# Kernel optimization log

Hardware: AMD Instinct MI355X
Metric: run time of the kernel (lower is better)

## Reference

```python
import jax, jax.numpy as jnp
import numpy as np

V, T, D, H, L, F, B = 50257, 1024, 1024, 16, 10, 4096, 2
HD = D // H  # head_dim = 64
EPS = 1e-5


def sinusoidal_pos(seq_len, d_model):
    pos = np.arange(seq_len)[:, None].astype(np.float32)
    i = np.arange(d_model // 2).astype(np.float32)
    inv = 1.0 / (10000.0 ** (2.0 * i / d_model))
    ang = pos * inv[None, :]
    pe = np.zeros((seq_len, d_model), dtype=np.float32)
    pe[:, 0::2] = np.sin(ang)
    pe[:, 1::2] = np.cos(ang)
    return jnp.asarray(pe)


def setup_inputs() -> dict:
    key = jax.random.key(0)
    ks = jax.random.split(key, 16)
    s = 0.02
    return {
        "x": jax.random.randint(ks[0], (B, T), 0, V),
        "emb": jax.random.normal(ks[1], (V, D), jnp.float32) * s,
        "pos": sinusoidal_pos(T, D),
        "Wq": jax.random.normal(ks[2], (L, D, D), jnp.float32) * s,
        "bq": jnp.zeros((L, D), jnp.float32),
        "Wk": jax.random.normal(ks[3], (L, D, D), jnp.float32) * s,
        "bk": jnp.zeros((L, D), jnp.float32),
        "Wv": jax.random.normal(ks[4], (L, D, D), jnp.float32) * s,
        "bv": jnp.zeros((L, D), jnp.float32),
        "ln_g": jnp.ones((L, D), jnp.float32),
        "ln_b": jnp.zeros((L, D), jnp.float32),
        "W1": jax.random.normal(ks[5], (L, D, F), jnp.float32) * s,
        "b1": jnp.zeros((L, F), jnp.float32),
        "W2": jax.random.normal(ks[6], (L, F, D), jnp.float32) * s,
        "b2": jnp.zeros((L, D), jnp.float32),
        "lnf_g": jnp.ones((D,), jnp.float32),
        "lnf_b": jnp.zeros((D,), jnp.float32),
        "Wout": jax.random.normal(ks[7], (D, V), jnp.float32) * s,
        "bout": jnp.zeros((V,), jnp.float32),
    }


def layer_norm(h, g, b):
    mu = jnp.mean(h, axis=-1, keepdims=True)
    var = jnp.mean(jnp.square(h - mu), axis=-1, keepdims=True)
    return (h - mu) * jax.lax.rsqrt(var + EPS) * g + b


def reference(x, emb, pos, Wq, bq, Wk, bk, Wv, bv, ln_g, ln_b, W1, b1, W2, b2, lnf_g, lnf_b, Wout, bout):
    t = x.shape[1]
    h = emb[x] + pos[None, :t]  # [B,T,D]
    causal = jnp.tril(jnp.ones((t, t), bool))  # True = keep
    scale = 1.0 / jnp.sqrt(jnp.float32(HD))

    def body(h, p):
        wq, bq_, wk, bk_, wv, bv_, g, bln, w1, b1_, w2, b2_ = p
        q = (h @ wq + bq_).reshape(B, t, H, HD)
        k = (h @ wk + bk_).reshape(B, t, H, HD)
        v = (h @ wv + bv_).reshape(B, t, H, HD)
        score = jnp.einsum('bqhd,bkhd->bhqk', q, k) * scale
        score = jnp.where(causal, score, -jnp.inf)
        attn = jax.nn.softmax(score, axis=-1)
        o = jnp.einsum('bhqk,bkhd->bqhd', attn, v).reshape(B, t, D)
        h = layer_norm(h + o, g, bln)
        m = jax.nn.gelu(h @ w1 + b1_, approximate=False) @ w2 + b2_
        h = layer_norm(h + m, g, bln)  # same LayerNorm params reused, as in source
        return h, None

    h, _ = jax.lax.scan(body, h, (Wq, bq, Wk, bk, Wv, bv, ln_g, ln_b, W1, b1, W2, b2))
    h = layer_norm(h, lnf_g, lnf_b)
    return h @ Wout + bout  # [B,T,V]
```

## Files before the change

### kernel.cpp

```cpp
#include <hip/hip_runtime.h>
#include <cstdint>
#include <cstddef>

#define Vv 50257
#define Va 50304
#define Tt 1024
#define Dd 1024
#define Hh 16
#define Ll 10
#define Ff 4096
#define Bb 2
#define Mm (Bb*Tt)

typedef float f32x4 __attribute__((ext_vector_type(4)));
typedef __bf16 bf16x8 __attribute__((ext_vector_type(8)));
typedef unsigned short u16x8 __attribute__((ext_vector_type(8)));
typedef unsigned short u16x4 __attribute__((ext_vector_type(4)));

static __device__ __forceinline__ unsigned short f2bf(float f) {
  unsigned int u = __builtin_bit_cast(unsigned int, f);
  unsigned int r = (u + 0x7FFFu + ((u >> 16) & 1u)) >> 16;
  return (unsigned short)r;
}

static __device__ __forceinline__ f32x4 mfma16x16x32(u16x8 a, u16x8 b, f32x4 c) {
  return __builtin_amdgcn_mfma_f32_16x16x32_bf16(
      __builtin_bit_cast(bf16x8, a), __builtin_bit_cast(bf16x8, b), c, 0, 0, 0);
}

static __device__ __forceinline__ void async_cp16(const void* g, void* l) {
  __builtin_amdgcn_global_load_lds(
      (const __attribute__((address_space(1))) unsigned int*)g,
      (__attribute__((address_space(3))) unsigned int*)l, 16, 0, 0);
}

__global__ __launch_bounds__(256) void embed_kernel(
    const int* __restrict__ x, const float* __restrict__ emb,
    const float* __restrict__ pos, float* __restrict__ h,
    unsigned short* __restrict__ hb) {
  int bt = blockIdx.x;
  int t = bt & (Tt - 1);
  int tok = x[bt];
  int i = threadIdx.x * 4;
  f32x4 e = *(const f32x4*)(emb + (size_t)tok * Dd + i);
  f32x4 p = *(const f32x4*)(pos + (size_t)t * Dd + i);
  f32x4 r = e + p;
  *(f32x4*)(h + (size_t)bt * Dd + i) = r;
  u16x4 rb = { f2bf(r[0]), f2bf(r[1]), f2bf(r[2]), f2bf(r[3]) };
  *(u16x4*)(hb + (size_t)bt * Dd + i) = rb;
}

__global__ __launch_bounds__(256) void add_ln_kernel(
    const float* __restrict__ hin, const float* __restrict__ r,
    const float* __restrict__ g, const float* __restrict__ bb,
    float* __restrict__ hout, unsigned short* __restrict__ hbout) {
  int row = blockIdx.x;
  int tid = threadIdx.x;
  size_t off = (size_t)row * Dd + tid * 4;
  f32x4 xv = *(const f32x4*)(hin + off);
  if (r) xv += *(const f32x4*)(r + off);
  float s  = xv[0] + xv[1] + xv[2] + xv[3];
  float ss = xv[0]*xv[0] + xv[1]*xv[1] + xv[2]*xv[2] + xv[3]*xv[3];
  #pragma unroll
  for (int o = 1; o < 64; o <<= 1) {
    s  += __shfl_xor(s, o);
    ss += __shfl_xor(ss, o);
  }
  __shared__ float red[8];
  int wave = tid >> 6, lane = tid & 63;
  if (lane == 0) { red[wave] = s; red[4 + wave] = ss; }
  __syncthreads();
  s  = red[0] + red[1] + red[2] + red[3];
  ss = red[4] + red[5] + red[6] + red[7];
  float mu = s * (1.0f / Dd);
  float var = ss * (1.0f / Dd) - mu * mu;
  float rstd = rsqrtf(var + 1e-5f);
  f32x4 gv = *(const f32x4*)(g + tid * 4);
  f32x4 bv = *(const f32x4*)(bb + tid * 4);
  f32x4 y;
  #pragma unroll
  for (int j = 0; j < 4; ++j) y[j] = (xv[j] - mu) * rstd * gv[j] + bv[j];
  *(f32x4*)(hout + off) = y;
  u16x4 yb = { f2bf(y[0]), f2bf(y[1]), f2bf(y[2]), f2bf(y[3]) };
  *(u16x4*)(hbout + off) = yb;
}

__global__ __launch_bounds__(256) void bias_gather_kernel(
    const float* __restrict__ bq, const float* __restrict__ bk,
    const float* __restrict__ bv, float* __restrict__ cb) {
  int l = blockIdx.x;
  int i = threadIdx.x * 4;
  f32x4 q = *(const f32x4*)(bq + (size_t)l * Dd + i);
  f32x4 k = *(const f32x4*)(bk + (size_t)l * Dd + i);
  f32x4 v = *(const f32x4*)(bv + (size_t)l * Dd + i);
  *(f32x4*)(cb + (size_t)l * 3072 + i) = q;
  *(f32x4*)(cb + (size_t)l * 3072 + 1024 + i) = k;
  *(f32x4*)(cb + (size_t)l * 3072 + 2048 + i) = v;
}

__global__ __launch_bounds__(256) void tconv_kernel(
    const float* __restrict__ W, unsigned short* __restrict__ Wt,
    int K, int N, int Nvalid, size_t sW, size_t sWt) {
  const float* Wl = W + (size_t)blockIdx.z * sW;
  unsigned short* Wtl = Wt + (size_t)blockIdx.z * sWt;
  __shared__ unsigned short t[64][72];
  int n0 = blockIdx.x * 64, k0 = blockIdx.y * 64;
  int tx = threadIdx.x & 15, ty = threadIdx.x >> 4;
  #pragma unroll
  for (int i = 0; i < 4; ++i) {
    int kr = ty + i * 16;
    int nc = tx * 4;
    int gn = n0 + nc;
    f32x4 v = {0.f, 0.f, 0.f, 0.f};
    if (gn + 3 < Nvalid) {
      v = *(const f32x4*)(Wl + (size_t)(k0 + kr) * N + gn);
    } else {
      #pragma unroll
      for (int j = 0; j < 4; ++j)
        if (gn + j < Nvalid) v[j] = Wl[(size_t)(k0 + kr) * N + gn + j];
    }
    t[nc + 0][kr] = f2bf(v[0]); t[nc + 1][kr] = f2bf(v[1]);
    t[nc + 2][kr] = f2bf(v[2]); t[nc + 3][kr] = f2bf(v[3]);
  }
  __syncthreads();
  #pragma unroll
  for (int i = 0; i < 4; ++i) {
    int nr = ty + i * 16;
    u16x4 o = *(const u16x4*)&t[nr][tx * 4];
    *(u16x4*)(Wtl + (size_t)(n0 + nr) * K + k0 + tx * 4) = o;
  }
}

template <int BM, int BN, int WR, int WC, int EPI, bool SWZ>
__global__ __launch_bounds__(256) void gemm_bt(
    const unsigned short* __restrict__ A, const unsigned short* __restrict__ Bt,
    const float* __restrict__ bias, void* __restrict__ Cout,
    int Ncols, int K) {
  static_assert(WR * WC == 4, "4 waves");
  constexpr int MI = BM / WR / 16;
  constexpr int NJ = BN / WC / 16;
  __shared__ __align__(16) unsigned short Al[2][BM * 32];
  __shared__ __align__(16) unsigned short Bl[2][BN * 32];
  int bx = blockIdx.x, by = blockIdx.y;
  if constexpr (SWZ) {
    unsigned gx = gridDim.x;
    unsigned total = gx * gridDim.y;
    unsigned flat = by * gx + bx;
    unsigned per = total >> 3;
    unsigned work = (flat & 7u) * per + (flat >> 3);
    bx = work % gx; by = work / gx;
  }
  const int bm = bx * BM;
  const int bn = by * BN;
  const int tid = threadIdx.x, lane = tid & 63, wave = tid >> 6;
  const int wm = (wave / WC) * (BM / WR);
  const int wn = (wave % WC) * (BN / WC);
  const int rowi = lane >> 2;
  const int koff = (lane & 3) * 8;

  auto stage = [&](int buf, int k0) {
    #pragma unroll
    for (int i = 0; i < BM / 64; ++i) {
      int ch = wave + i * 4;
      async_cp16(A + (size_t)(bm + ch * 16 + rowi) * K + k0 + koff, &Al[buf][ch * 512]);
    }
    #pragma unroll
    for (int i = 0; i < BN / 64; ++i) {
      int ch = wave + i * 4;
      async_cp16(Bt + (size_t)(bn + ch * 16 + rowi) * K + k0 + koff, &Bl[buf][ch * 512]);
    }
  };

  f32x4 acc[MI][NJ];
  #pragma unroll
  for (int i = 0; i < MI; ++i)
    #pragma unroll
    for (int j = 0; j < NJ; ++j) acc[i][j] = {0.f, 0.f, 0.f, 0.f};

  stage(0, 0);
  __syncthreads();
  int cur = 0;
  for (int k0 = 0; k0 < K; k0 += 32) {
    if (k0 + 32 < K) stage(cur ^ 1, k0 + 32);
    u16x8 af[MI], bfr[NJ];
    #pragma unroll
    for (int i = 0; i < MI; ++i)
      af[i] = *(const u16x8*)&Al[cur][(wm + i * 16 + (lane & 15)) * 32 + (lane >> 4) * 8];
    #pragma unroll
    for (int j = 0; j < NJ; ++j)
      bfr[j] = *(const u16x8*)&Bl[cur][(wn + j * 16 + (lane & 15)) * 32 + (lane >> 4) * 8];
    #pragma unroll
    for (int i = 0; i < MI; ++i)
      #pragma unroll
      for (int j = 0; j < NJ; ++j)
        acc[i][j] = mfma16x16x32(af[i], bfr[j], acc[i][j]);
    __syncthreads();
    cur ^= 1;
  }

  float bvv[NJ];
  #pragma unroll
  for (int j = 0; j < NJ; ++j) {
    int col = bn + wn + j * 16 + (lane & 15);
    bvv[j] = (col < Ncols) ? bias[col] : 0.0f;
  }
  #pragma unroll
  for (int i = 0; i < MI; ++i) {
    #pragma unroll
    for (int rr = 0; rr < 4; ++rr) {
      int row = bm + wm + i * 16 + (lane >> 4) * 4 + rr;
      #pragma unroll
      for (int j = 0; j < NJ; ++j) {
        int col = bn + wn + j * 16 + (lane & 15);
        if (col < Ncols) {
          float val = acc[i][j][rr] + bvv[j];
          if constexpr (EPI == 0) {
            ((float*)Cout)[(size_t)row * Ncols + col] = val;
          } else if constexpr (EPI == 1) {
            ((unsigned short*)Cout)[(size_t)row * Ncols + col] = f2bf(val);
          } else {
            float gv = 0.5f * val * (1.0f + erff(val * 0.70710678f));
            ((unsigned short*)Cout)[(size_t)row * Ncols + col] = f2bf(gv);
          }
        }
      }
    }
  }
}

template <int EPI>
__global__ __launch_bounds__(256) void gemm_f32b(
    const unsigned short* __restrict__ A, const float* __restrict__ Bw,
    const float* __restrict__ bias, void* __restrict__ Cout, int N, int K) {
  __shared__ __align__(16) unsigned short Al[128][40];
  __shared__ __align__(16) unsigned short Btl[128][40];
  const int bn = blockIdx.x * 128;
  const int bm = blockIdx.y * 128;
  const int tid = threadIdx.x;
  const int lane = tid & 63;
  const int wave = tid >> 6;
  const int wm = (wave >> 1) * 64;
  const int wn = (wave & 1) * 64;
  const bool nfast = ((N & 3) == 0);

  f32x4 acc[4][4];
  #pragma unroll
  for (int i = 0; i < 4; ++i)
    #pragma unroll
    for (int j = 0; j < 4; ++j) acc[i][j] = {0.f, 0.f, 0.f, 0.f};

  for (int k0 = 0; k0 < K; k0 += 32) {
    __syncthreads();
    #pragma unroll
    for (int i = 0; i < 2; ++i) {
      int c = tid + i * 256;
      int row = c >> 2, ko = (c & 3) * 8;
      u16x8 v = *(const u16x8*)(A + (size_t)(bm + row) * K + k0 + ko);
      *(u16x8*)&Al[row][ko] = v;
    }
    if (nfast) {
      #pragma unroll
      for (int i = 0; i < 4; ++i) {
        int c = tid + i * 256;
        int kr = c >> 5;
        int no = (c & 31) * 4;
        f32x4 v4 = *(const f32x4*)(Bw + (size_t)(k0 + kr) * N + bn + no);
        Btl[no + 0][kr] = f2bf(v4[0]); Btl[no + 1][kr] = f2bf(v4[1]);
        Btl[no + 2][kr] = f2bf(v4[2]); Btl[no + 3][kr] = f2bf(v4[3]);
      }
    } else {
      #pragma unroll
      for (int i = 0; i < 4; ++i) {
        int c = tid + i * 256;
        int kr = c >> 5;
        int nb = c & 31;
        #pragma unroll
        for (int j = 0; j < 4; ++j) {
          int col = nb + j * 32;
          float v = (bn + col < N) ? Bw[(size_t)(k0 + kr) * N + bn + col] : 0.0f;
          Btl[col][kr] = f2bf(v);
        }
      }
    }
    __syncthreads();
    u16x8 af[4], bfr[4];
    #pragma unroll
    for (int i = 0; i < 4; ++i)
      af[i] = *(const u16x8*)&Al[wm + i * 16 + (lane & 15)][(lane >> 4) * 8];
    #pragma unroll
    for (int j = 0; j < 4; ++j)
      bfr[j] = *(const u16x8*)&Btl[wn + j * 16 + (lane & 15)][(lane >> 4) * 8];
    #pragma unroll
    for (int i = 0; i < 4; ++i)
      #pragma unroll
      for (int j = 0; j < 4; ++j)
        acc[i][j] = mfma16x16x32(af[i], bfr[j], acc[i][j]);
  }
  #pragma unroll
  for (int j = 0; j < 4; ++j) {
    int col = bn + wn + j * 16 + (lane & 15);
    bool cok = (col < N);
    float bv = cok ? bias[col] : 0.0f;
    #pragma unroll
    for (int i = 0; i < 4; ++i) {
      #pragma unroll
      for (int rr = 0; rr < 4; ++rr) {
        int row = bm + wm + i * 16 + (lane >> 4) * 4 + rr;
        float val = acc[i][j][rr] + bv;
        if (cok) {
          if constexpr (EPI == 0) ((float*)Cout)[(size_t)row * N + col] = val;
          else if constexpr (EPI == 1) ((unsigned short*)Cout)[(size_t)row * N + col] = f2bf(val);
          else {
            float gv = 0.5f * val * (1.0f + erff(val * 0.70710678f));
            ((unsigned short*)Cout)[(size_t)row * N + col] = f2bf(gv);
          }
        }
      }
    }
  }
}

__global__ __launch_bounds__(256) void attn_kernel(
    const unsigned short* __restrict__ q, const unsigned short* __restrict__ k,
    const unsigned short* __restrict__ v, float* __restrict__ o, int ld) {
  const int ys = blockIdx.y;
  const int qt = (ys < 8) ? ys : 23 - ys;
  const int bh = blockIdx.x;
  const int b = bh >> 4, h = bh & 15;
  const size_t base = (size_t)b * Tt * ld + (size_t)h * 64;
  const int tid = threadIdx.x, lane = tid & 63, wave = tid >> 6;
  const int q0 = qt * 64 + wave * 16;

  __shared__ __align__(16) unsigned short Kl[64][72];
  __shared__ __align__(16) unsigned short Vt[64][72];
  __shared__ __align__(16) unsigned short Pl[4][16][72];

  const float SC = 0.18033688011112042f;

  u16x8 qa[2];
  {
    const unsigned short* qp = q + base + (size_t)(q0 + (lane & 15)) * ld + (lane >> 4) * 8;
    qa[0] = *(const u16x8*)qp;
    qa[1] = *(const u16x8*)(qp + 32);
  }

  f32x4 Oacc[4];
  #pragma unroll
  for (int df = 0; df < 4; ++df) Oacc[df] = {0.f, 0.f, 0.f, 0.f};
  float m_run[4], l_run[4];
  #pragma unroll
  for (int rr = 0; rr < 4; ++rr) { m_run[rr] = -__builtin_inff(); l_run[rr] = 0.f; }

  for (int kt = 0; kt <= qt; ++kt) {
    __syncthreads();
    #pragma unroll
    for (int i = 0; i < 2; ++i) {
      int c = tid + i * 256;
      int rr = c >> 3, dof = (c & 7) * 8;
      *(u16x8*)&Kl[rr][dof] =
          *(const u16x8*)(k + base + (size_t)(kt * 64 + rr) * ld + dof);
    }
    #pragma unroll
    for (int i = 0; i < 2; ++i) {
      int c = tid + i * 256;
      int rr = c >> 3, dof = (c & 7) * 8;
      u16x8 vv = *(const u16x8*)(v + base + (size_t)(kt * 64 + rr) * ld + dof);
      #pragma unroll
      for (int j = 0; j < 8; ++j) {
        int d = dof + j;
        Vt[d][(rr + (d & 56)) & 63] = vv[j];
      }
    }
    __syncthreads();

    f32x4 S[4];
    #pragma unroll
    for (int nf = 0; nf < 4; ++nf) {
      S[nf] = {0.f, 0.f, 0.f, 0.f};
      #pragma unroll
      for (int s = 0; s < 2; ++s) {
        u16x8 kb = *(const u16x8*)&Kl[nf * 16 + (lane & 15)][s * 32 + (lane >> 4) * 8];
        S[nf] = mfma16x16x32(qa[s], kb, S[nf]);
      }
    }
    const int kbase = kt * 64;
    float mx[4];
    #pragma unroll
    for (int rr = 0; rr < 4; ++rr) mx[rr] = -__builtin_inff();
    #pragma unroll
    for (int nf = 0; nf < 4; ++nf) {
      int kcol = kbase + nf * 16 + (lane & 15);
      #pragma unroll
      for (int rr = 0; rr < 4; ++rr) {
        int qrow = q0 + (lane >> 4) * 4 + rr;
        float sv = S[nf][rr] * SC;
        if (kcol > qrow) sv = -__builtin_inff();
        S[nf][rr] = sv;
        mx[rr] = fmaxf(mx[rr], sv);
      }
    }
    #pragma unroll
    for (int rr = 0; rr < 4; ++rr) {
      #pragma unroll
      for (int off = 1; off < 16; off <<= 1)
        mx[rr] = fmaxf(mx[rr], __shfl_xor(mx[rr], off));
    }
    float psum[4];
    #pragma unroll
    for (int rr = 0; rr < 4; ++rr) {
      float mnew = fmaxf(m_run[rr], mx[rr]);
      float sc = exp2f(m_run[rr] - mnew);
      l_run[rr] *= sc;
      #pragma unroll
      for (int df = 0; df < 4; ++df) Oacc[df][rr] *= sc;
      m_run[rr] = mnew;
      psum[rr] = 0.f;
    }
    #pragma unroll
    for (int nf = 0; nf < 4; ++nf) {
      #pragma unroll
      for (int rr = 0; rr < 4; ++rr) {
        float pv = exp2f(S[nf][rr] - m_run[rr]);
        S[nf][rr] = pv;
        psum[rr] += pv;
      }
    }
    #pragma unroll
    for (int rr = 0; rr < 4; ++rr) {
      #pragma unroll
      for (int off = 1; off < 16; off <<= 1) psum[rr] += __shfl_xor(psum[rr], off);
      l_run[rr] += psum[rr];
    }
    #pragma unroll
    for (int nf = 0; nf < 4; ++nf)
      #pragma unroll
      for (int rr = 0; rr < 4; ++rr)
        Pl[wave][(lane >> 4) * 4 + rr][nf * 16 + (lane & 15)] = f2bf(S[nf][rr]);
    __syncthreads();
    #pragma unroll
    for (int s = 0; s < 2; ++s) {
      u16x8 pa = *(const u16x8*)&Pl[wave][lane & 15][s * 32 + (lane >> 4) * 8];
      #pragma unroll
      for (int df = 0; df < 4; ++df) {
        int d = df * 16 + (lane & 15);
        int cs = (s * 32 + (lane >> 4) * 8 + (d & 56)) & 63;
        u16x8 vb = *(const u16x8*)&Vt[d][cs];
        Oacc[df] = mfma16x16x32(pa, vb, Oacc[df]);
      }
    }
  }

  #pragma unroll
  for (int df = 0; df < 4; ++df) {
    int d = df * 16 + (lane & 15);
    #pragma unroll
    for (int rr = 0; rr < 4; ++rr) {
      int qrow = q0 + (lane >> 4) * 4 + rr;
      o[((size_t)b * Tt + qrow) * Dd + h * 64 + d] = Oacc[df][rr] / l_run[rr];
    }
  }
}

extern "C" void kernel_launch(void* const* d_in, const int* in_sizes, int n_in,
                              void* d_out, int out_size, void* d_ws, size_t ws_size,
                              hipStream_t stream) {
  const int*   x     = (const int*)d_in[0];
  const float* emb   = (const float*)d_in[1];
  const float* pos   = (const float*)d_in[2];
  const float* Wq    = (const float*)d_in[3];
  const float* bq    = (const float*)d_in[4];
  const float* Wk    = (const float*)d_in[5];
  const float* bk    = (const float*)d_in[6];
  const float* Wv    = (const float*)d_in[7];
  const float* bv    = (const float*)d_in[8];
  const float* ln_g  = (const float*)d_in[9];
  const float* ln_b  = (const float*)d_in[10];
  const float* W1    = (const float*)d_in[11];
  const float* b1    = (const float*)d_in[12];
  const float* W2    = (const float*)d_in[13];
  const float* b2    = (const float*)d_in[14];
  const float* lnf_g = (const float*)d_in[15];
  const float* lnf_b = (const float*)d_in[16];
  const float* Wout  = (const float*)d_in[17];
  const float* bout  = (const float*)d_in[18];
  float* out = (float*)d_out;

  char* p = (char*)d_ws;
  auto alloc = [&](size_t bytes) {
    char* r = p; p += (bytes + 255) & ~(size_t)255; return r;
  };
  float* h           = (float*)alloc((size_t)Mm * Dd * 4);
  unsigned short* hb = (unsigned short*)alloc((size_t)Mm * Dd * 2);
  unsigned short* qkv = (unsigned short*)alloc((size_t)Mm * 3072 * 2);
  float* of          = (float*)alloc((size_t)Mm * Dd * 4);
  unsigned short* a1 = (unsigned short*)alloc((size_t)Mm * Ff * 2);
  float* cb          = (float*)alloc((size_t)Ll * 3072 * 4);
  size_t base_used = (size_t)(p - (char*)d_ws);

  const size_t SZ_WQKVT = (size_t)Ll * 3072 * Dd * 2;
  const size_t SZ_W1T   = (size_t)Ll * Ff * Dd * 2;
  const size_t SZ_W2T   = (size_t)Ll * Dd * Ff * 2;
  const size_t SZ_WOUTT = (size_t)Va * Dd * 2;
  const size_t need_big = base_used + SZ_WQKVT + SZ_W1T + SZ_W2T + SZ_WOUTT + 4096;
  const size_t need_rot = base_used + SZ_WOUTT + 4096;

  embed_kernel<<<Mm, 256, 0, stream>>>(x, emb, pos, h, hb);

  if (ws_size >= need_rot) {
    bias_gather_kernel<<<Ll, 256, 0, stream>>>(bq, bk, bv, cb);
    const bool big = (ws_size >= need_big);
    unsigned short *wqkvt, *w1t, *w2t, *woutt;
    if (big) {
      wqkvt = (unsigned short*)alloc(SZ_WQKVT);
      w1t   = (unsigned short*)alloc(SZ_W1T);
      w2t   = (unsigned short*)alloc(SZ_W2T);
      woutt = (unsigned short*)alloc(SZ_WOUTT);
      tconv_kernel<<<dim3(16, 16, Ll), 256, 0, stream>>>(
          Wq, wqkvt,           Dd, Dd, Dd, (size_t)Dd*Dd, (size_t)3072*Dd);
      tconv_kernel<<<dim3(16, 16, Ll), 256, 0, stream>>>(
          Wk, wqkvt + 1024*Dd, Dd, Dd, Dd, (size_t)Dd*Dd, (size_t)3072*Dd);
      tconv_kernel<<<dim3(16, 16, Ll), 256, 0, stream>>>(
          Wv, wqkvt + 2048*Dd, Dd, Dd, Dd, (size_t)Dd*Dd, (size_t)3072*Dd);
      tconv_kernel<<<dim3(Ff/64, Dd/64, Ll), 256, 0, stream>>>(
          W1, w1t, Dd, Ff, Ff, (size_t)Dd*Ff, (size_t)Ff*Dd);
      tconv_kernel<<<dim3(Dd/64, Ff/64, Ll), 256, 0, stream>>>(
          W2, w2t, Ff, Dd, Dd, (size_t)Ff*Dd, (size_t)Dd*Ff);
      tconv_kernel<<<dim3(Va/64, Dd/64, 1), 256, 0, stream>>>(
          Wout, woutt, Dd, Vv, Vv, 0, 0);
    } else {
      unsigned short* wbuf = (unsigned short*)alloc(SZ_WOUTT);
      wqkvt = w1t = w2t = woutt = wbuf;
    }

    for (int l = 0; l < Ll; ++l) {
      unsigned short* wq_l = big ? (wqkvt + (size_t)l * 3072 * Dd) : wqkvt;
      if (!big) {
        tconv_kernel<<<dim3(16, 16, 1), 256, 0, stream>>>(Wq + (size_t)l * Dd * Dd, wq_l,           Dd, Dd, Dd, 0, 0);
        tconv_kernel<<<dim3(16, 16, 1), 256, 0, stream>>>(Wk + (size_t)l * Dd * Dd, wq_l + 1024*Dd, Dd, Dd, Dd, 0, 0);
        tconv_kernel<<<dim3(16, 16, 1), 256, 0, stream>>>(Wv + (size_t)l * Dd * Dd, wq_l + 2048*Dd, Dd, Dd, Dd, 0, 0);
      }
      gemm_bt<64, 128, 1, 4, 1, false><<<dim3(Mm/64, 3072/128), 256, 0, stream>>>(
          hb, wq_l, cb + (size_t)l * 3072, qkv, 3072, Dd);
      attn_kernel<<<dim3(Bb*Hh, Tt/64), 256, 0, stream>>>(qkv, qkv + 1024, qkv + 2048, of, 3072);
      add_ln_kernel<<<Mm, 256, 0, stream>>>(h, of, ln_g + (size_t)l * Dd,
                                            ln_b + (size_t)l * Dd, h, hb);
      unsigned short* w1_l = big ? (w1t + (size_t)l * Ff * Dd) : w1t;
      if (!big)
        tconv_kernel<<<dim3(Ff/64, Dd/64, 1), 256, 0, stream>>>(W1 + (size_t)l * Dd * Ff, w1_l, Dd, Ff, Ff, 0, 0);
      gemm_bt<128, 128, 2, 2, 2, false><<<dim3(Mm/128, Ff/128), 256, 0, stream>>>(
          hb, w1_l, b1 + (size_t)l * Ff, a1, Ff, Dd);
      unsigned short* w2_l = big ? (w2t + (size_t)l * Dd * Ff) : w2t;
      if (!big)
        tconv_kernel<<<dim3(Dd/64, Ff/64, 1), 256, 0, stream>>>(W2 + (size_t)l * Ff * Dd, w2_l, Ff, Dd, Dd, 0, 0);
      gemm_bt<64, 128, 1, 4, 0, false><<<dim3(Mm/64, Dd/128), 256, 0, stream>>>(
          a1, w2_l, b2 + (size_t)l * Dd, of, Dd, Ff);
      add_ln_kernel<<<Mm, 256, 0, stream>>>(h, of, ln_g + (size_t)l * Dd,
                                            ln_b + (size_t)l * Dd, h, hb);
    }

    add_ln_kernel<<<Mm, 256, 0, stream>>>(h, nullptr, lnf_g, lnf_b, h, hb);
    if (!big)
      tconv_kernel<<<dim3(Va/64, Dd/64, 1), 256, 0, stream>>>(Wout, woutt, Dd, Vv, Vv, 0, 0);
    gemm_bt<128, 128, 2, 2, 0, true><<<dim3(Mm/128, Va/128), 256, 0, stream>>>(
        hb, woutt, bout, out, Vv, Dd);
  } else {
    unsigned short* qb = qkv;
    unsigned short* kb = qkv + (size_t)Mm * Dd;
    unsigned short* vb = qkv + (size_t)2 * Mm * Dd;
    for (int l = 0; l < Ll; ++l) {
      const size_t wo = (size_t)l * Dd * Dd;
      gemm_f32b<1><<<dim3(Dd/128, Mm/128), 256, 0, stream>>>(hb, Wq + wo, bq + (size_t)l*Dd, qb, Dd, Dd);
      gemm_f32b<1><<<dim3(Dd/128, Mm/128), 256, 0, stream>>>(hb, Wk + wo, bk + (size_t)l*Dd, kb, Dd, Dd);
      gemm_f32b<1><<<dim3(Dd/128, Mm/128), 256, 0, stream>>>(hb, Wv + wo, bv + (size_t)l*Dd, vb, Dd, Dd);
      attn_kernel<<<dim3(Bb*Hh, Tt/64), 256, 0, stream>>>(qb, kb, vb, of, Dd);
      add_ln_kernel<<<Mm, 256, 0, stream>>>(h, of, ln_g + (size_t)l*Dd, ln_b + (size_t)l*Dd, h, hb);
      gemm_f32b<2><<<dim3(Ff/128, Mm/128), 256, 0, stream>>>(hb, W1 + (size_t)l*Dd*Ff, b1 + (size_t)l*Ff, a1, Ff, Dd);
      gemm_f32b<0><<<dim3(Dd/128, Mm/128), 256, 0, stream>>>(a1, W2 + (size_t)l*Ff*Dd, b2 + (size_t)l*Dd, of, Dd, Ff);
      add_ln_kernel<<<Mm, 256, 0, stream>>>(h, of, ln_g + (size_t)l*Dd, ln_b + (size_t)l*Dd, h, hb);
    }
    add_ln_kernel<<<Mm, 256, 0, stream>>>(h, nullptr, lnf_g, lnf_b, h, hb);
    gemm_f32b<0><<<dim3((Vv + 127)/128, Mm/128), 256, 0, stream>>>(hb, Wout, bout, out, Vv, Dd);
  }
}
```

Measured before the change: 2.552 ms.

## Split-K the W2 GEMM and fuse partial reduction into add+LayerNorm

The FFN down-projection GEMM (K=4096, N=1024) now runs with a split-K of 4 over a third grid dimension. Each slice writes fp32 partial sums to a new workspace buffer, and a new add+LayerNorm kernel sums the partials and the b2 bias before normalizing. This is meant to fill more CUs, since the original grid had only 256 tiles and a long K loop. The QKV GEMM also moves from 64x128 to 128x128 tiles. The cost is 4x fp32 partial-output traffic (about 32MB written and read per layer) and larger workspace.

```diff
diff --git a/kernel.cpp b/kernel.cpp
--- a/kernel.cpp
+++ b/kernel.cpp
@@ -11,6 +11,7 @@
 #define Ff 4096
 #define Bb 2
 #define Mm (Bb*Tt)
+#define KSPLIT 4
 
 typedef float f32x4 __attribute__((ext_vector_type(4)));
 typedef __bf16 bf16x8 __attribute__((ext_vector_type(8)));
@@ -85,6 +86,45 @@
   *(u16x4*)(hbout + off) = yb;
 }
 
+__global__ __launch_bounds__(256) void add_ln_red_kernel(
+    const float* __restrict__ hin, const float* __restrict__ parts,
+    const float* __restrict__ bias2,
+    const float* __restrict__ g, const float* __restrict__ bb,
+    float* __restrict__ hout, unsigned short* __restrict__ hbout) {
+  int row = blockIdx.x;
+  int tid = threadIdx.x;
+  size_t off = (size_t)row * Dd + tid * 4;
+  f32x4 xv = *(const f32x4*)(hin + off);
+  xv += *(const f32x4*)(bias2 + tid * 4);
+  #pragma unroll
+  for (int s = 0; s < KSPLIT; ++s)
+    xv += *(const f32x4*)(parts + (size_t)s * Mm * Dd + off);
+  float s  = xv[0] + xv[1] + xv[2] + xv[3];
+  float ss = xv[0]*xv[0] + xv[1]*xv[1] + xv[2]*xv[2] + xv[3]*xv[3];
+  #pragma unroll
+  for (int o = 1; o < 64; o <<= 1) {
+    s  += __shfl_xor(s, o);
+    ss += __shfl_xor(ss, o);
+  }
+  __shared__ float red[8];
+  int wave = tid >> 6, lane = tid & 63;
+  if (lane == 0) { red[wave] = s; red[4 + wave] = ss; }
+  __syncthreads();
+  s  = red[0] + red[1] + red[2] + red[3];
+  ss = red[4] + red[5] + red[6] + red[7];
+  float mu = s * (1.0f / Dd);
+  float var = ss * (1.0f / Dd) - mu * mu;
+  float rstd = rsqrtf(var + 1e-5f);
+  f32x4 gv = *(const f32x4*)(g + tid * 4);
+  f32x4 bv = *(const f32x4*)(bb + tid * 4);
+  f32x4 y;
+  #pragma unroll
+  for (int j = 0; j < 4; ++j) y[j] = (xv[j] - mu) * rstd * gv[j] + bv[j];
+  *(f32x4*)(hout + off) = y;
+  u16x4 yb = { f2bf(y[0]), f2bf(y[1]), f2bf(y[2]), f2bf(y[3]) };
+  *(u16x4*)(hbout + off) = yb;
+}
+
 __global__ __launch_bounds__(256) void bias_gather_kernel(
     const float* __restrict__ bq, const float* __restrict__ bk,
     const float* __restrict__ bv, float* __restrict__ cb) {
@@ -131,11 +171,11 @@
   }
 }
 
-template <int BM, int BN, int WR, int WC, int EPI, bool SWZ>
+template <int BM, int BN, int WR, int WC, int EPI, bool SWZ, int KS>
 __global__ __launch_bounds__(256) void gemm_bt(
     const unsigned short* __restrict__ A, const unsigned short* __restrict__ Bt,
     const float* __restrict__ bias, void* __restrict__ Cout,
-    int Ncols, int K) {
+    int Ncols, int K, size_t zstr) {
   static_assert(WR * WC == 4, "4 waves");
   constexpr int MI = BM / WR / 16;
   constexpr int NJ = BN / WC / 16;
@@ -177,11 +217,14 @@
     #pragma unroll
     for (int j = 0; j < NJ; ++j) acc[i][j] = {0.f, 0.f, 0.f, 0.f};
 
-  stage(0, 0);
+  const int kbeg = (KS > 1) ? (int)blockIdx.z * (K / KS) : 0;
+  const int kend = kbeg + K / KS;
+
+  stage(0, kbeg);
   __syncthreads();
   int cur = 0;
-  for (int k0 = 0; k0 < K; k0 += 32) {
-    if (k0 + 32 < K) stage(cur ^ 1, k0 + 32);
+  for (int k0 = kbeg; k0 < kend; k0 += 32) {
+    if (k0 + 32 < kend) stage(cur ^ 1, k0 + 32);
     u16x8 af[MI], bfr[NJ];
     #pragma unroll
     for (int i = 0; i < MI; ++i)
@@ -201,9 +244,12 @@
   float bvv[NJ];
   #pragma unroll
   for (int j = 0; j < NJ; ++j) {
-    int col = bn + wn + j * 16 + (lane & 15);
-    bvv[j] = (col < Ncols) ? bias[col] : 0.0f;
-  }
+    if constexpr (EPI != 3) {
+      int col = bn + wn + j * 16 + (lane & 15);
+      bvv[j] = (col < Ncols) ? bias[col] : 0.0f;
+    } else bvv[j] = 0.0f;
+  }
+  float* Cz = (EPI == 3) ? ((float*)Cout + (size_t)blockIdx.z * zstr) : (float*)Cout;
   #pragma unroll
   for (int i = 0; i < MI; ++i) {
     #pragma unroll
@@ -218,9 +264,11 @@
             ((float*)Cout)[(size_t)row * Ncols + col] = val;
           } else if constexpr (EPI == 1) {
             ((unsigned short*)Cout)[(size_t)row * Ncols + col] = f2bf(val);
-          } else {
+          } else if constexpr (EPI == 2) {
             float gv = 0.5f * val * (1.0f + erff(val * 0.70710678f));
             ((unsigned short*)Cout)[(size_t)row * Ncols + col] = f2bf(gv);
+          } else {
+            Cz[(size_t)row * Ncols + col] = val;
           }
         }
       }
@@ -495,6 +543,7 @@
   float* of          = (float*)alloc((size_t)Mm * Dd * 4);
   unsigned short* a1 = (unsigned short*)alloc((size_t)Mm * Ff * 2);
   float* cb          = (float*)alloc((size_t)Ll * 3072 * 4);
+  float* parts       = (float*)alloc((size_t)KSPLIT * Mm * Dd * 4);
   size_t base_used = (size_t)(p - (char*)d_ws);
 
   const size_t SZ_WQKVT = (size_t)Ll * 3072 * Dd * 2;
@@ -539,30 +588,31 @@
         tconv_kernel<<<dim3(16, 16, 1), 256, 0, stream>>>(Wk + (size_t)l * Dd * Dd, wq_l + 1024*Dd, Dd, Dd, Dd, 0, 0);
         tconv_kernel<<<dim3(16, 16, 1), 256, 0, stream>>>(Wv + (size_t)l * Dd * Dd, wq_l + 2048*Dd, Dd, Dd, Dd, 0, 0);
       }
-      gemm_bt<64, 128, 1, 4, 1, false><<<dim3(Mm/64, 3072/128), 256, 0, stream>>>(
-          hb, wq_l, cb + (size_t)l * 3072, qkv, 3072, Dd);
+      gemm_bt<128, 128, 2, 2, 1, false, 1><<<dim3(Mm/128, 3072/128), 256, 0, stream>>>(
+          hb, wq_l, cb + (size_t)l * 3072, qkv, 3072, Dd, 0);
       attn_kernel<<<dim3(Bb*Hh, Tt/64), 256, 0, stream>>>(qkv, qkv + 1024, qkv + 2048, of, 3072);
       add_ln_kernel<<<Mm, 256, 0, stream>>>(h, of, ln_g + (size_t)l * Dd,
                                             ln_b + (size_t)l * Dd, h, hb);
       unsigned short* w1_l = big ? (w1t + (size_t)l * Ff * Dd) : w1t;
       if (!big)
         tconv_kernel<<<dim3(Ff/64, Dd/64, 1), 256, 0, stream>>>(W1 + (size_t)l * Dd * Ff, w1_l, Dd, Ff, Ff, 0, 0);
-      gemm_bt<128, 128, 2, 2, 2, false><<<dim3(Mm/128, Ff/128), 256, 0, stream>>>(
-          hb, w1_l, b1 + (size_t)l * Ff, a1, Ff, Dd);
+      gemm_bt<128, 128, 2, 2, 2, false, 1><<<dim3(Mm/128, Ff/128), 256, 0, stream>>>(
+          hb, w1_l, b1 + (size_t)l * Ff, a1, Ff, Dd, 0);
       unsigned short* w2_l = big ? (w2t + (size_t)l * Dd * Ff) : w2t;
       if (!big)
         tconv_kernel<<<dim3(Dd/64, Ff/64, 1), 256, 0, stream>>>(W2 + (size_t)l * Ff * Dd, w2_l, Ff, Dd, Dd, 0, 0);
-      gemm_bt<64, 128, 1, 4, 0, false><<<dim3(Mm/64, Dd/128), 256, 0, stream>>>(
-          a1, w2_l, b2 + (size_t)l * Dd, of, Dd, Ff);
-      add_ln_kernel<<<Mm, 256, 0, stream>>>(h, of, ln_g + (size_t)l * Dd,
-                                            ln_b + (size_t)l * Dd, h, hb);
+      gemm_bt<128, 128, 2, 2, 3, false, KSPLIT><<<dim3(Mm/128, Dd/128, KSPLIT), 256, 0, stream>>>(
+          a1, w2_l, nullptr, parts, Dd, Ff, (size_t)Mm * Dd);
+      add_ln_red_kernel<<<Mm, 256, 0, stream>>>(h, parts, b2 + (size_t)l * Dd,
+                                                ln_g + (size_t)l * Dd,
+                                                ln_b + (size_t)l * Dd, h, hb);
     }
 
     add_ln_kernel<<<Mm, 256, 0, stream>>>(h, nullptr, lnf_g, lnf_b, h, hb);
     if (!big)
       tconv_kernel<<<dim3(Va/64, Dd/64, 1), 256, 0, stream>>>(Wout, woutt, Dd, Vv, Vv, 0, 0);
-    gemm_bt<128, 128, 2, 2, 0, true><<<dim3(Mm/128, Va/128), 256, 0, stream>>>(
-        hb, woutt, bout, out, Vv, Dd);
+    gemm_bt<128, 128, 2, 2, 0, true, 1><<<dim3(Mm/128, Va/128), 256, 0, stream>>>(
+        hb, woutt, bout, out, Vv, Dd, 0);
   } else {
     unsigned short* qb = qkv;
     unsigned short* kb = qkv + (size_t)Mm * Dd;
```

Result: faster. 2.324 ms (-8.9%).
